# Kernel optimization log

Hardware: AMD Instinct MI355X
Metric: run time of the kernel (lower is better)

Reference implementation:

```python
import jax, jax.numpy as jnp
import numpy as np

B = 64            # graphs
N0 = 1024         # nodes per graph at level 0
DEG = 16          # avg degree
D = 128
NS = [1024, 820, 656, 525, 420, 336]  # ceil(0.8*n) cascade


def gcn(x, src, dst, valid, W, b, num_nodes):
    # x: [N,D]; src/dst: [E] int; valid: [E] float mask; W: [D,D]; b: [D]
    x = x @ W.T + b
    deg = jax.ops.segment_sum(valid, src, num_segments=num_nodes) + 1.0  # +1 self loop
    dis = jax.lax.rsqrt(deg)
    norm = dis[src] * dis[dst] * valid
    agg = jax.ops.segment_sum(norm[:, None] * x[src], dst, num_segments=num_nodes)
    return agg + (dis * dis)[:, None] * x  # self-loop term


def topk_pool(x, src, dst, valid, w, n, k):
    # PyG TopKPooling: score = tanh((x.w)/||w||); keep top ceil(ratio*n) per graph
    s = jnp.tanh((x @ w) / jnp.linalg.norm(w))
    _, idx = jax.lax.top_k(s.reshape(B, n), k)                    # [B,k] local ids
    perm = (idx + (jnp.arange(B) * n)[:, None]).reshape(-1)       # global ids
    xn = x[perm] * s[perm][:, None]
    new_id = jnp.full((B * n,), -1, jnp.int32).at[perm].set(jnp.arange(B * k, dtype=jnp.int32))
    ns_, nd_ = new_id[src], new_id[dst]
    v = valid * ((ns_ >= 0) & (nd_ >= 0)).astype(jnp.float32)
    return xn, jnp.maximum(ns_, 0), jnp.maximum(nd_, 0), v


def setup_inputs() -> dict:
    key = jax.random.key(0)
    ks = jax.random.split(key, 32)
    x = jax.random.normal(ks[0], (B * N0, D), jnp.float32)
    eg = N0 * DEG  # edges per graph
    local = jax.random.randint(ks[1], (2, B, eg), 0, N0, jnp.int32)
    edge_index = (local + (jnp.arange(B, dtype=jnp.int32) * N0)[None, :, None]).reshape(2, -1)
    batch = jnp.repeat(jnp.arange(B, dtype=jnp.int32), N0)
    sc = 1.0 / np.sqrt(D)
    inp = {"x": x, "edge_index": edge_index, "batch": batch}
    for i in range(1, 6):
        inp[f"c{i}w"] = jax.random.normal(ks[2 * i], (D, D), jnp.float32) * sc
        inp[f"c{i}b"] = jnp.zeros((D,), jnp.float32)
        inp[f"p{i}w"] = jax.random.normal(ks[2 * i + 1], (D,), jnp.float32) * sc
    inp["l1w"] = jax.random.normal(ks[20], (128, 256), jnp.float32) / np.sqrt(256)
    inp["l1b"] = jnp.zeros((128,), jnp.float32)
    inp["l2w"] = jax.random.normal(ks[21], (64, 128), jnp.float32) * sc
    inp["l2b"] = jnp.zeros((64,), jnp.float32)
    inp["l3w"] = jax.random.normal(ks[22], (2, 64), jnp.float32) / np.sqrt(64)
    inp["l3b"] = jnp.zeros((2,), jnp.float32)
    return inp


def reference(x, edge_index, batch,
              c1w, c1b, p1w, c2w, c2b, p2w, c3w, c3b, p3w,
              c4w, c4b, p4w, c5w, c5b, p5w,
              l1w, l1b, l2w, l2b, l3w, l3b):
    src, dst = edge_index[0], edge_index[1]
    valid = jnp.ones(src.shape, jnp.float32)
    layers = [(c1w, c1b, p1w), (c2w, c2b, p2w), (c3w, c3b, p3w),
              (c4w, c4b, p4w), (c5w, c5b, p5w)]
    reads = []
    for i, (cw, cb, pw) in enumerate(layers):
        n, k = NS[i], NS[i + 1]
        x = jax.nn.relu(gcn(x, src, dst, valid, cw, cb, B * n))
        x, src, dst, valid = topk_pool(x, src, dst, valid, pw, n, k)
        xk = x.reshape(B, k, D)
        reads.append(jnp.concatenate([xk.max(axis=1), xk.mean(axis=1)], axis=1))
    h = reads[0] + reads[1] + reads[2] + reads[3] + reads[4]   # [B,256]
    h = jax.nn.relu(h @ l1w.T + l1b)
    # dropout is identity in eval mode
    h = jax.nn.relu(h @ l2w.T + l2b)
    return jax.nn.log_softmax(h @ l3w.T + l3b, axis=-1)       # [B,2]
```

## Files before the change

### kernel.cpp

```cpp
#include <hip/hip_runtime.h>
#include <hip/hip_fp16.h>
#include <math.h>

#define NB 64
#define DIM 128
#define ETOT 1048576
#define EPG 16384
#define EPT 16
#define WRS 192
#define XRS 96

static const int NS_H[6] = {1024, 820, 656, 525, 420, 336};

__device__ __forceinline__ unsigned fxform(float f) {
    int b = __float_as_int(f);
    return (b >= 0) ? ((unsigned)b | 0x80000000u) : ~(unsigned)b;
}
__device__ __forceinline__ float fxinv(unsigned u) {
    int b = (u & 0x80000000u) ? (int)(u ^ 0x80000000u) : (int)~u;
    return __int_as_float(b);
}

__global__ __launch_bounds__(1024) void init_kernel(const int* __restrict__ ei,
                                  int* __restrict__ src, int* __restrict__ dst,
                                  int2* __restrict__ epack, int* __restrict__ eoff,
                                  int* __restrict__ cnt, float* __restrict__ dinv,
                                  float* __restrict__ invn, const float* __restrict__ pw0,
                                  unsigned* __restrict__ maxb, float* __restrict__ sumb) {
    __shared__ int hs[1024], hc[1024], cur[1024];
    __shared__ float dv[1024];
    __shared__ float shf[128];
    __shared__ int wsum[16];
    int g = blockIdx.x, t = threadIdx.x;
    int lane = t & 63, wv = t >> 6;
    hs[t] = 0; hc[t] = 0;
    int idx = g * 1024 + t;
    if (idx < 5 * NB * 128) { maxb[idx] = 0x007FFFFFu; sumb[idx] = 0.f; }
    __syncthreads();
    int b0 = g * EPG;
    int sr[EPT], dr[EPT];
#pragma unroll
    for (int q = 0; q < EPT; q++) {
        int e = b0 + q * 1024 + t;
        int s = ei[e], d = ei[ETOT + e];
        sr[q] = s; dr[q] = d;
        src[e] = s; dst[e] = d;
        atomicAdd(&hs[s & 1023], 1);
        atomicAdd(&hc[d & 1023], 1);
    }
    __syncthreads();
    int v = hc[t];
    dv[t] = rsqrtf((float)hs[t] + 1.0f);
    int s = v;
#pragma unroll
    for (int off = 1; off < 64; off <<= 1) {
        int u = __shfl_up(s, off, 64);
        if (lane >= off) s += u;
    }
    if (lane == 63) wsum[wv] = s;
    __syncthreads();
    if (wv == 0) {
        int ws = (lane < 16) ? wsum[lane] : 0;
#pragma unroll
        for (int off = 1; off < 16; off <<= 1) {
            int u = __shfl_up(ws, off, 64);
            if (lane >= off) ws += u;
        }
        if (lane < 16) wsum[lane] = ws;
    }
    __syncthreads();
    int excl = b0 + s + ((wv > 0) ? wsum[wv - 1] : 0) - v;
    eoff[g * 1024 + t] = excl;
    cnt[g * 1024 + t] = v;
    dinv[g * 1024 + t] = dv[t];
    cur[t] = excl;
    __syncthreads();
#pragma unroll
    for (int q = 0; q < EPT; q++) {
        int sl = sr[q] & 1023, dl = dr[q] & 1023;
        int pos = atomicAdd(&cur[dl], 1);
        epack[pos] = make_int2(sr[q], __float_as_int(dv[sl] * dv[dl]));
    }
    if (g == 0) {
        if (t < 128) shf[t] = pw0[t] * pw0[t];
        __syncthreads();
        for (int q = 64; q > 0; q >>= 1) {
            if (t < q) shf[t] += shf[t + q];
            __syncthreads();
        }
        if (t == 0) invn[0] = rsqrtf(shf[0]);
    }
}

__global__ __launch_bounds__(256) void linear_kernel(const float* __restrict__ x,
                              const __half* __restrict__ xA,
                              const int* __restrict__ perm, const float* __restrict__ sval,
                              const float* __restrict__ W, const float* __restrict__ b,
                              __half* __restrict__ xH,
                              unsigned* __restrict__ maxbL, float* __restrict__ sumbL,
                              int n_prev, int kk, int cpg, int mode) {
    __shared__ float Wt[32 * WRS];
    __shared__ float xT[32 * XRS];
    __shared__ float rmax[128], rsum[128];
    __shared__ float rmax2[8][32], rsum2[8][32];
    int tid = threadIdx.x;
    int g   = blockIdx.x / cpg;
    int j0  = (blockIdx.x % cpg) * 64;
    int nf = tid & 15;
    int u  = tid >> 4;
    int r   = tid & 63;
    int dq2 = tid >> 6;
    int jrow = j0 + r;
    int rowg = 0; float sscale = 1.f; bool valid = true;
    if (mode) {
        valid = (jrow < kk);
        int idx = g * kk + (valid ? jrow : 0);
        rowg = perm[idx];
        sscale = sval[idx];
    }
    float acc[4][8];
    {
        float bv[8];
#pragma unroll
        for (int f = 0; f < 8; f++) bv[f] = b[u * 8 + f];
#pragma unroll
        for (int i = 0; i < 4; i++)
#pragma unroll
            for (int f = 0; f < 8; f++) acc[i][f] = bv[f];
    }
    for (int kb = 0; kb < 4; kb++) {
        __syncthreads();
#pragma unroll
        for (int q = 0; q < 4; q++) {
            int i = q * 256 + tid;
            int dq = i >> 7;
            int rr = i & 127;
            int s = (rr >> 3) * 12 + (rr & 7);
            float4 wv = *(const float4*)(W + rr * 128 + kb * 32 + dq * 4);
            Wt[(dq * 4 + 0) * WRS + s] = wv.x;
            Wt[(dq * 4 + 1) * WRS + s] = wv.y;
            Wt[(dq * 4 + 2) * WRS + s] = wv.z;
            Wt[(dq * 4 + 3) * WRS + s] = wv.w;
        }
        int s = (r >> 3) * 12 + (r & 7);
        if (mode) {
            uint4 hv = *(const uint4*)(xA + ((size_t)(g * n_prev + rowg)) * DIM + kb * 32 + dq2 * 8);
            float2 c0 = __half22float2(*(const __half2*)&hv.x);
            float2 c1 = __half22float2(*(const __half2*)&hv.y);
            float2 c2 = __half22float2(*(const __half2*)&hv.z);
            float2 c3 = __half22float2(*(const __half2*)&hv.w);
            float v[8] = {c0.x * sscale, c0.y * sscale, c1.x * sscale, c1.y * sscale,
                          c2.x * sscale, c2.y * sscale, c3.x * sscale, c3.y * sscale};
            int cb2 = dq2 * 8;
#pragma unroll
            for (int i = 0; i < 8; i++) xT[(cb2 + i) * XRS + s] = valid ? v[i] : 0.f;
        } else {
#pragma unroll
            for (int q = 0; q < 2; q++) {
                int i = q * 256 + tid;
                int dq = i >> 6;
                float4 xv = *(const float4*)(x + (size_t)(g * kk + jrow) * DIM + kb * 32 + dq * 4);
                xT[(dq * 4 + 0) * XRS + s] = xv.x;
                xT[(dq * 4 + 1) * XRS + s] = xv.y;
                xT[(dq * 4 + 2) * XRS + s] = xv.z;
                xT[(dq * 4 + 3) * XRS + s] = xv.w;
            }
        }
        __syncthreads();
        if (mode) {
            int col = tid & 31, grp = tid >> 5;
            float m = -INFINITY, sv2 = 0.f;
#pragma unroll
            for (int rr = 0; rr < 8; rr++) {
                int ro = (rr + col) & 7;
                int row = grp * 8 + ro;
                float v = xT[col * XRS + grp * 12 + ro];
                if (j0 + row < kk) m = fmaxf(m, v);
                sv2 += v;
            }
            rmax2[grp][col] = m;
            rsum2[grp][col] = sv2;
        }
        __syncthreads();
        if (mode && tid < 32) {
            float m = rmax2[0][tid], sv2 = rsum2[0][tid];
#pragma unroll
            for (int p = 1; p < 8; p++) {
                m = fmaxf(m, rmax2[p][tid]);
                sv2 += rsum2[p][tid];
            }
            rmax[kb * 32 + tid] = m;
            rsum[kb * 32 + tid] = sv2;
        }
#pragma unroll 4
        for (int d = 0; d < 32; d++) {
            float4 xv = *(const float4*)&xT[d * XRS + (nf >> 1) * 12 + (nf & 1) * 4];
            float4 wa = *(const float4*)&Wt[d * WRS + u * 12];
            float4 wb = *(const float4*)&Wt[d * WRS + u * 12 + 4];
            float xs[4] = {xv.x, xv.y, xv.z, xv.w};
            float ws[8] = {wa.x, wa.y, wa.z, wa.w, wb.x, wb.y, wb.z, wb.w};
#pragma unroll
            for (int i = 0; i < 4; i++)
#pragma unroll
                for (int f = 0; f < 8; f++)
                    acc[i][f] += xs[i] * ws[f];
        }
    }
#pragma unroll
    for (int i = 0; i < 4; i++) {
        int jl = nf * 4 + i;
        if (j0 + jl < kk) {
            int nd = g * kk + j0 + jl;
            alignas(16) __half2 hb[4];
            hb[0] = __floats2half2_rn(acc[i][0], acc[i][1]);
            hb[1] = __floats2half2_rn(acc[i][2], acc[i][3]);
            hb[2] = __floats2half2_rn(acc[i][4], acc[i][5]);
            hb[3] = __floats2half2_rn(acc[i][6], acc[i][7]);
            *(float4*)(xH + (size_t)nd * DIM + u * 8) = *(const float4*)hb;
        }
    }
    if (mode) {
        __syncthreads();
        if (tid < 128) {
            atomicMax(&maxbL[g * 128 + tid], fxform(rmax[tid]));
            atomicAdd(&sumbL[g * 128 + tid], rsum[tid]);
        }
    }
}

#define CVT8_FMA(xv, wg) { \
    float2 c0_ = __half22float2(*(const __half2*)&(xv).x); \
    float2 c1_ = __half22float2(*(const __half2*)&(xv).y); \
    float2 c2_ = __half22float2(*(const __half2*)&(xv).z); \
    float2 c3_ = __half22float2(*(const __half2*)&(xv).w); \
    acc0 += (wg) * c0_.x; acc1 += (wg) * c0_.y; acc2 += (wg) * c1_.x; acc3 += (wg) * c1_.y; \
    acc4 += (wg) * c2_.x; acc5 += (wg) * c2_.y; acc6 += (wg) * c3_.x; acc7 += (wg) * c3_.y; }

__global__ __launch_bounds__(256, 4) void fused_agg_kernel(
                                 const __half* __restrict__ xH, const int2* __restrict__ epack,
                                 const int* __restrict__ eoff, const int* __restrict__ cnt,
                                 const float* __restrict__ dinv,
                                 const float* __restrict__ pw, const float* __restrict__ invn,
                                 __half* __restrict__ xA, float* __restrict__ score, int n) {
    int t = threadIdx.x;
    int g = blockIdx.x % NB;
    int chunk = blockIdx.x / NB;
    int ln = chunk * 8 + (t >> 5);
    if (ln >= n) return;
    int node = g * n + ln;
    int lane = t & 31;
    int sub = lane & 15;
    int hi  = lane >> 4;
    const uint4* __restrict__ xr = (const uint4*)xH;
    float dsn = dinv[node];
    float acc0 = 0.f, acc1 = 0.f, acc2 = 0.f, acc3 = 0.f;
    float acc4 = 0.f, acc5 = 0.f, acc6 = 0.f, acc7 = 0.f;
    {
        uint4 qs = xr[(unsigned)node * 16u + sub];
        float w0 = hi ? 0.f : dsn * dsn;
        CVT8_FMA(qs, w0);
    }
    int s0 = eoff[node], s1 = s0 + cnt[node];
    int j = s0;
    if ((j & 1) && j < s1) {
        int2 eq = epack[j];
        float wg = hi ? 0.f : __int_as_float(eq.y);
        uint4 xv = xr[(unsigned)eq.x * 16u + sub];
        CVT8_FMA(xv, wg);
        j++;
    }
    int np = (s1 - j) >> 1;
    int odd = (s1 - j) & 1;
    const int4* __restrict__ ep2 = (const int4*)epack;
    int p = j >> 1;
    while (np >= 8) {
        int4 E0 = ep2[p + 0], E1 = ep2[p + 1], E2 = ep2[p + 2], E3 = ep2[p + 3];
        int4 E4 = ep2[p + 4], E5 = ep2[p + 5], E6 = ep2[p + 6], E7 = ep2[p + 7];
        unsigned r0 = (unsigned)(hi ? E0.z : E0.x); float w0_ = __int_as_float(hi ? E0.w : E0.y);
        unsigned r1 = (unsigned)(hi ? E1.z : E1.x); float w1_ = __int_as_float(hi ? E1.w : E1.y);
        unsigned r2 = (unsigned)(hi ? E2.z : E2.x); float w2_ = __int_as_float(hi ? E2.w : E2.y);
        unsigned r3 = (unsigned)(hi ? E3.z : E3.x); float w3_ = __int_as_float(hi ? E3.w : E3.y);
        unsigned r4 = (unsigned)(hi ? E4.z : E4.x); float w4_ = __int_as_float(hi ? E4.w : E4.y);
        unsigned r5 = (unsigned)(hi ? E5.z : E5.x); float w5_ = __int_as_float(hi ? E5.w : E5.y);
        unsigned r6 = (unsigned)(hi ? E6.z : E6.x); float w6_ = __int_as_float(hi ? E6.w : E6.y);
        unsigned r7 = (unsigned)(hi ? E7.z : E7.x); float w7_ = __int_as_float(hi ? E7.w : E7.y);
        uint4 x0 = xr[r0 * 16u + sub];
        uint4 x1 = xr[r1 * 16u + sub];
        uint4 x2 = xr[r2 * 16u + sub];
        uint4 x3 = xr[r3 * 16u + sub];
        uint4 x4 = xr[r4 * 16u + sub];
        uint4 x5 = xr[r5 * 16u + sub];
        uint4 x6 = xr[r6 * 16u + sub];
        uint4 x7 = xr[r7 * 16u + sub];
        CVT8_FMA(x0, w0_); CVT8_FMA(x1, w1_); CVT8_FMA(x2, w2_); CVT8_FMA(x3, w3_);
        CVT8_FMA(x4, w4_); CVT8_FMA(x5, w5_); CVT8_FMA(x6, w6_); CVT8_FMA(x7, w7_);
        p += 8; np -= 8;
    }
    if (np >= 4) {
        int4 E0 = ep2[p + 0], E1 = ep2[p + 1], E2 = ep2[p + 2], E3 = ep2[p + 3];
        unsigned r0 = (unsigned)(hi ? E0.z : E0.x); float w0_ = __int_as_float(hi ? E0.w : E0.y);
        unsigned r1 = (unsigned)(hi ? E1.z : E1.x); float w1_ = __int_as_float(hi ? E1.w : E1.y);
        unsigned r2 = (unsigned)(hi ? E2.z : E2.x); float w2_ = __int_as_float(hi ? E2.w : E2.y);
        unsigned r3 = (unsigned)(hi ? E3.z : E3.x); float w3_ = __int_as_float(hi ? E3.w : E3.y);
        uint4 x0 = xr[r0 * 16u + sub];
        uint4 x1 = xr[r1 * 16u + sub];
        uint4 x2 = xr[r2 * 16u + sub];
        uint4 x3 = xr[r3 * 16u + sub];
        CVT8_FMA(x0, w0_); CVT8_FMA(x1, w1_); CVT8_FMA(x2, w2_); CVT8_FMA(x3, w3_);
        p += 4; np -= 4;
    }
    for (; np > 0; np--, p++) {
        int4 E = ep2[p];
        uint4 xv = xr[(unsigned)(hi ? E.z : E.x) * 16u + sub];
        float wg = __int_as_float(hi ? E.w : E.y);
        CVT8_FMA(xv, wg);
    }
    if (odd) {
        int2 eq = epack[s1 - 1];
        float wg = hi ? 0.f : __int_as_float(eq.y);
        uint4 xv = xr[(unsigned)eq.x * 16u + sub];
        CVT8_FMA(xv, wg);
    }
    acc0 += __shfl_xor(acc0, 16, 32); acc1 += __shfl_xor(acc1, 16, 32);
    acc2 += __shfl_xor(acc2, 16, 32); acc3 += __shfl_xor(acc3, 16, 32);
    acc4 += __shfl_xor(acc4, 16, 32); acc5 += __shfl_xor(acc5, 16, 32);
    acc6 += __shfl_xor(acc6, 16, 32); acc7 += __shfl_xor(acc7, 16, 32);
    acc0 = fmaxf(acc0, 0.f); acc1 = fmaxf(acc1, 0.f);
    acc2 = fmaxf(acc2, 0.f); acc3 = fmaxf(acc3, 0.f);
    acc4 = fmaxf(acc4, 0.f); acc5 = fmaxf(acc5, 0.f);
    acc6 = fmaxf(acc6, 0.f); acc7 = fmaxf(acc7, 0.f);
    if (!hi) {
        __half2 h0 = __floats2half2_rn(acc0, acc1);
        __half2 h1 = __floats2half2_rn(acc2, acc3);
        __half2 h2 = __floats2half2_rn(acc4, acc5);
        __half2 h3 = __floats2half2_rn(acc6, acc7);
        uint4 pk;
        pk.x = *(unsigned int*)&h0; pk.y = *(unsigned int*)&h1;
        pk.z = *(unsigned int*)&h2; pk.w = *(unsigned int*)&h3;
        ((uint4*)xA)[(unsigned)node * 16u + sub] = pk;
    }
    float4 pa = ((const float4*)pw)[sub * 2];
    float4 pb = ((const float4*)pw)[sub * 2 + 1];
    float dot = acc0 * pa.x + acc1 * pa.y + acc2 * pa.z + acc3 * pa.w
              + acc4 * pb.x + acc5 * pb.y + acc6 * pb.z + acc7 * pb.w;
#pragma unroll
    for (int off = 8; off >= 1; off >>= 1) dot += __shfl_xor(dot, off, 16);
    if (lane == 0) score[node] = tanhf(dot * invn[0]);
}

__global__ __launch_bounds__(1024) void pool_kernel(const float* __restrict__ score,
                              int* __restrict__ permG, float* __restrict__ svalG,
                              int* __restrict__ src, int* __restrict__ dst,
                              int2* __restrict__ epack, int* __restrict__ eoff,
                              int* __restrict__ cnt, float* __restrict__ dinv,
                              const float* __restrict__ pwN, float* __restrict__ invn,
                              int n, int k, int last) {
    __shared__ float keyS[2][1024];
    __shared__ int idxS[2][1024];
    __shared__ int nid[1024];
    __shared__ int hs[1024], hc[1024], cur[1024];
    __shared__ float dv[1024];
    __shared__ float shf[128];
    __shared__ int wsum[16];
    int g = blockIdx.x, t = threadIdx.x;
    int lane = t & 63, wv = t >> 6;
    int b0 = g * EPG, gn = g * n, gk = g * k;
    float k_r = (t < n) ? score[g * n + t] : -2.0f;
    int i_r = t;
    hs[t] = 0; hc[t] = 0;
    int se[EPT], de[EPT];
    if (!last) {
#pragma unroll
        for (int q = 0; q < EPT; q++) {
            int e = b0 + q * 1024 + t;
            se[q] = src[e];
            de[q] = dst[e];
        }
    }
    int par = 0;
    for (unsigned ksz = 2; ksz <= 1024; ksz <<= 1) {
        for (unsigned jj = ksz >> 1; jj > 0; jj >>= 1) {
            float kq; int iq;
            if (jj >= 64) {
                keyS[par][t] = k_r; idxS[par][t] = i_r;
                __syncthreads();
                kq = keyS[par][t ^ jj]; iq = idxS[par][t ^ jj];
                par ^= 1;
            } else {
                kq = __shfl_xor(k_r, (int)jj, 64);
                iq = __shfl_xor(i_r, (int)jj, 64);
            }
            bool mineFirst = (k_r > kq) || (k_r == kq && i_r < iq);
            bool up = ((t & ksz) == 0);
            bool iAmLower = ((t & jj) == 0);
            bool keepMine = (iAmLower == up) ? mineFirst : !mineFirst;
            if (!keepMine) { k_r = kq; i_r = iq; }
        }
    }
    nid[i_r] = (t < (unsigned)k) ? t : -1;
    if (t < k) { permG[gk + t] = i_r; svalG[gk + t] = k_r; }
    __syncthreads();
    if (last) return;
    int sr[EPT], dr[EPT];
#pragma unroll
    for (int q = 0; q < EPT; q++) {
        int e = b0 + q * 1024 + t;
        int s = se[q];
        int s2 = -1, d2 = -1;
        if (s >= 0) {
            s2 = nid[s - gn];
            d2 = nid[de[q] - gn];
            if (s2 >= 0 && d2 >= 0) {
                src[e] = gk + s2;
                dst[e] = gk + d2;
                atomicAdd(&hs[s2], 1);
                atomicAdd(&hc[d2], 1);
            } else {
                src[e] = -1;
                dst[e] = -1;
                s2 = -1;
            }
        }
        sr[q] = s2; dr[q] = d2;
    }
    __syncthreads();
    int v = (t < k) ? hc[t] : 0;
    if (t < k) dv[t] = rsqrtf((float)hs[t] + 1.0f);
    int s = v;
#pragma unroll
    for (int off = 1; off < 64; off <<= 1) {
        int u = __shfl_up(s, off, 64);
        if (lane >= off) s += u;
    }
    if (lane == 63) wsum[wv] = s;
    __syncthreads();
    if (wv == 0) {
        int ws = (lane < 16) ? wsum[lane] : 0;
#pragma unroll
        for (int off = 1; off < 16; off <<= 1) {
            int u = __shfl_up(ws, off, 64);
            if (lane >= off) ws += u;
        }
        if (lane < 16) wsum[lane] = ws;
    }
    __syncthreads();
    if (t < k) {
        int excl = b0 + s + ((wv > 0) ? wsum[wv - 1] : 0) - v;
        eoff[gk + t] = excl;
        cnt[gk + t] = v;
        dinv[gk + t] = dv[t];
        cur[t] = excl;
    }
    __syncthreads();
#pragma unroll
    for (int q = 0; q < EPT; q++) {
        if (sr[q] >= 0) {
            int pos = atomicAdd(&cur[dr[q]], 1);
            epack[pos] = make_int2(gk + sr[q], __float_as_int(dv[sr[q]] * dv[dr[q]]));
        }
    }
    if (g == 0) {
        if (t < 128) shf[t] = pwN[t] * pwN[t];
        __syncthreads();
        for (int q = 64; q > 0; q >>= 1) {
            if (t < q) shf[t] += shf[t + q];
            __syncthreads();
        }
        if (t == 0) invn[0] = rsqrtf(shf[0]);
    }
}

__global__ __launch_bounds__(256) void gather_kernel(const __half* __restrict__ xA,
                                const int* __restrict__ permG, const float* __restrict__ svalG,
                                unsigned* __restrict__ maxbL, float* __restrict__ sumbL,
                                int n, int k) {
    __shared__ float4 smx[8][33];
    __shared__ float4 ssm[8][33];
    int t = threadIdx.x;
    int g = blockIdx.x % NB;
    int chunk = blockIdx.x / NB;
    int j = chunk * 8 + (t >> 5);
    int lane = t & 31;
    int ch = t >> 5;
    float4 mx = make_float4(-INFINITY, -INFINITY, -INFINITY, -INFINITY);
    float4 sm = make_float4(0.f, 0.f, 0.f, 0.f);
    if (j < k) {
        int row = permG[g * k + j];
        float s = svalG[g * k + j];
        uint2 hv = ((const uint2*)(xA + ((size_t)g * n + row) * DIM))[lane];
        float2 lo = __half22float2(*(const __half2*)&hv.x);
        float2 hi = __half22float2(*(const __half2*)&hv.y);
        float4 vv = make_float4(lo.x * s, lo.y * s, hi.x * s, hi.y * s);
        mx = vv; sm = vv;
    }
    smx[ch][lane] = mx;
    ssm[ch][lane] = sm;
    __syncthreads();
    for (int s = 4; s >= 1; s >>= 1) {
        if (ch < s) {
            float4 a = smx[ch][lane], bb = smx[ch + s][lane];
            a.x = fmaxf(a.x, bb.x); a.y = fmaxf(a.y, bb.y);
            a.z = fmaxf(a.z, bb.z); a.w = fmaxf(a.w, bb.w);
            smx[ch][lane] = a;
            float4 c = ssm[ch][lane], d = ssm[ch + s][lane];
            c.x += d.x; c.y += d.y; c.z += d.z; c.w += d.w;
            ssm[ch][lane] = c;
        }
        __syncthreads();
    }
    if (ch == 0) {
        float4 m = smx[0][lane];
        float4 s4 = ssm[0][lane];
        int f0 = g * 128 + lane * 4;
        atomicMax(&maxbL[f0 + 0], fxform(m.x));
        atomicMax(&maxbL[f0 + 1], fxform(m.y));
        atomicMax(&maxbL[f0 + 2], fxform(m.z));
        atomicMax(&maxbL[f0 + 3], fxform(m.w));
        atomicAdd(&sumbL[f0 + 0], s4.x);
        atomicAdd(&sumbL[f0 + 1], s4.y);
        atomicAdd(&sumbL[f0 + 2], s4.z);
        atomicAdd(&sumbL[f0 + 3], s4.w);
    }
}

__global__ __launch_bounds__(128) void head_kernel(const unsigned* __restrict__ maxb,
                              const float* __restrict__ sumb,
                              const float* __restrict__ l1w, const float* __restrict__ l1b,
                              const float* __restrict__ l2w, const float* __restrict__ l2b,
                              const float* __restrict__ l3w, const float* __restrict__ l3b,
                              float* __restrict__ out) {
    __shared__ float hr[256], h1[128], h2[64], lz[2];
    int g = blockIdx.x, t = threadIdx.x;
    const float invk[5] = {1.f / 820.f, 1.f / 656.f, 1.f / 525.f, 1.f / 420.f, 1.f / 336.f};
    float mxs = 0.f, sms = 0.f;
#pragma unroll
    for (int L = 0; L < 5; L++) {
        mxs += fxinv(maxb[(L * NB + g) * 128 + t]);
        sms += sumb[(L * NB + g) * 128 + t] * invk[L];
    }
    hr[t] = mxs;
    hr[128 + t] = sms;
    __syncthreads();
    float a1 = l1b[t];
    for (int d = 0; d < 256; d++) a1 += hr[d] * l1w[t * 256 + d];
    h1[t] = fmaxf(a1, 0.f);
    __syncthreads();
    if (t < 64) {
        float a2 = l2b[t];
        for (int d = 0; d < 128; d++) a2 += h1[d] * l2w[t * 128 + d];
        h2[t] = fmaxf(a2, 0.f);
    }
    __syncthreads();
    if (t < 2) {
        float a3 = l3b[t];
        for (int d = 0; d < 64; d++) a3 += h2[d] * l3w[t * 64 + d];
        lz[t] = a3;
    }
    __syncthreads();
    if (t < 2) {
        float z0 = lz[0], z1 = lz[1];
        float m = fmaxf(z0, z1);
        float lse = m + logf(expf(z0 - m) + expf(z1 - m));
        out[g * 2 + t] = lz[t] - lse;
    }
}

extern "C" void kernel_launch(void* const* d_in, const int* in_sizes, int n_in,
                              void* d_out, int out_size, void* d_ws, size_t ws_size,
                              hipStream_t stream) {
    const float* x_in = (const float*)d_in[0];
    const int* edge_index = (const int*)d_in[1];
    const float *cw[5], *cb[5], *pw[5];
    for (int i = 0; i < 5; i++) {
        cw[i] = (const float*)d_in[3 + 3 * i];
        cb[i] = (const float*)d_in[4 + 3 * i];
        pw[i] = (const float*)d_in[5 + 3 * i];
    }
    const float* l1w = (const float*)d_in[18];
    const float* l1b = (const float*)d_in[19];
    const float* l2w = (const float*)d_in[20];
    const float* l2b = (const float*)d_in[21];
    const float* l3w = (const float*)d_in[22];
    const float* l3b = (const float*)d_in[23];
    float* out = (float*)d_out;

    char* w = (char*)d_ws;
    __half* xA    = (__half*)w; w += (size_t)65536 * DIM * 2;
    __half* xH    = (__half*)w; w += (size_t)65536 * DIM * 2;
    int*   src   = (int*)w;   w += (size_t)ETOT * 4;
    int*   dst   = (int*)w;   w += (size_t)ETOT * 4;
    int2*  epack = (int2*)w;  w += (size_t)ETOT * 8;
    int*   cnt   = (int*)w;   w += (size_t)65536 * 4;
    int*   eoff  = (int*)w;   w += (size_t)65536 * 4;
    float* dinv  = (float*)w; w += (size_t)65536 * 4;
    float* score = (float*)w; w += (size_t)65536 * 4;
    int*   perm  = (int*)w;   w += (size_t)65536 * 4;
    float* sval  = (float*)w; w += (size_t)65536 * 4;
    unsigned* maxb = (unsigned*)w; w += (size_t)5 * NB * 128 * 4;
    float* sumb  = (float*)w; w += (size_t)5 * NB * 128 * 4;
    float* invn  = (float*)w; w += 4;

    init_kernel<<<NB, 1024, 0, stream>>>(edge_index, src, dst, epack, eoff, cnt, dinv,
                                         invn, pw[0], maxb, sumb);

    for (int i = 0; i < 5; i++) {
        int n = NS_H[i], k = NS_H[i + 1];
        int cpg = (n + 63) / 64;
        int last = (i == 4) ? 1 : 0;

        linear_kernel<<<NB * cpg, 256, 0, stream>>>(
            x_in, xA, perm, sval, cw[i], cb[i], xH,
            (i > 0) ? maxb + (size_t)(i - 1) * NB * 128 : (unsigned*)maxb,
            (i > 0) ? sumb + (size_t)(i - 1) * NB * 128 : (float*)sumb,
            (i > 0) ? NS_H[i - 1] : 0, n, cpg, (i > 0) ? 1 : 0);

        int gpb = (n + 7) / 8;
        fused_agg_kernel<<<NB * gpb, 256, 0, stream>>>(xH, epack, eoff, cnt, dinv, pw[i],
                                                       invn, xA, score, n);
        pool_kernel<<<NB, 1024, 0, stream>>>(score, perm, sval, src, dst, epack, eoff,
                                             cnt, dinv, (i < 4) ? pw[i + 1] : pw[i], invn,
                                             n, k, last);
    }
    int k4 = NS_H[5];
    int gpk = (k4 + 7) / 8;
    gather_kernel<<<NB * gpk, 256, 0, stream>>>(xA, perm, sval,
                                                maxb + (size_t)4 * NB * 128,
                                                sumb + (size_t)4 * NB * 128,
                                                NS_H[4], k4);
    head_kernel<<<NB, 128, 0, stream>>>(maxb, sumb, l1w, l1b, l2w, l2b, l3w, l3b, out);
}
```

Measured before the change: 505.8 us.

## Use fp16 MFMA for GCN linear layer with shuffle-based readout reduction

Replaces the FP32 LDS-tiled outer-product GEMM in linear_kernel with the 16x16x32 fp16 MFMA instruction. Weights are converted to fp16 once in init_kernel, and activations are loaded straight into registers as B fragments. The per-block max/mean readout now uses cross-lane shuffles in half precision instead of LDS transposes. This removes LDS staging and most syncs, but the input x and the scaled activations are rounded to fp16, and partial sums are accumulated in fp16 during the shuffle steps, which costs accuracy.

```diff
diff --git a/kernel.cpp b/kernel.cpp
--- a/kernel.cpp
+++ b/kernel.cpp
@@ -7,10 +7,11 @@
 #define ETOT 1048576
 #define EPG 16384
 #define EPT 16
-#define WRS 192
-#define XRS 96
 
 static const int NS_H[6] = {1024, 820, 656, 525, 420, 336};
+
+typedef _Float16 f16x8 __attribute__((ext_vector_type(8)));
+typedef float f32x4 __attribute__((ext_vector_type(4)));
 
 __device__ __forceinline__ unsigned fxform(float f) {
     int b = __float_as_int(f);
@@ -19,6 +20,18 @@
 __device__ __forceinline__ float fxinv(unsigned u) {
     int b = (u & 0x80000000u) ? (int)(u ^ 0x80000000u) : (int)~u;
     return __int_as_float(b);
+}
+__device__ __forceinline__ unsigned hmax2u(unsigned a, unsigned b) {
+    float2 fa = __half22float2(*(__half2*)&a);
+    float2 fb = __half22float2(*(__half2*)&b);
+    __half2 r = __floats2half2_rn(fmaxf(fa.x, fb.x), fmaxf(fa.y, fb.y));
+    return *(unsigned*)&r;
+}
+__device__ __forceinline__ unsigned hadd2u(unsigned a, unsigned b) {
+    float2 fa = __half22float2(*(__half2*)&a);
+    float2 fb = __half22float2(*(__half2*)&b);
+    __half2 r = __floats2half2_rn(fa.x + fb.x, fa.y + fb.y);
+    return *(unsigned*)&r;
 }
 
 __global__ __launch_bounds__(1024) void init_kernel(const int* __restrict__ ei,
@@ -26,7 +39,10 @@
                                   int2* __restrict__ epack, int* __restrict__ eoff,
                                   int* __restrict__ cnt, float* __restrict__ dinv,
                                   float* __restrict__ invn, const float* __restrict__ pw0,
-                                  unsigned* __restrict__ maxb, float* __restrict__ sumb) {
+                                  unsigned* __restrict__ maxb, float* __restrict__ sumb,
+                                  const float* __restrict__ cw0, const float* __restrict__ cw1,
+                                  const float* __restrict__ cw2, const float* __restrict__ cw3,
+                                  const float* __restrict__ cw4, __half* __restrict__ W16) {
     __shared__ int hs[1024], hc[1024], cur[1024];
     __shared__ float dv[1024];
     __shared__ float shf[128];
@@ -36,6 +52,12 @@
     hs[t] = 0; hc[t] = 0;
     int idx = g * 1024 + t;
     if (idx < 5 * NB * 128) { maxb[idx] = 0x007FFFFFu; sumb[idx] = 0.f; }
+    if (g < 5) {
+        const float* wsrc = (g == 0) ? cw0 : (g == 1) ? cw1 : (g == 2) ? cw2
+                           : (g == 3) ? cw3 : cw4;
+        for (int i = t; i < 16384; i += 1024)
+            W16[g * 16384 + i] = __float2half(wsrc[i]);
+    }
     __syncthreads();
     int b0 = g * EPG;
     int sr[EPT], dr[EPT];
@@ -95,135 +117,126 @@
 __global__ __launch_bounds__(256) void linear_kernel(const float* __restrict__ x,
                               const __half* __restrict__ xA,
                               const int* __restrict__ perm, const float* __restrict__ sval,
-                              const float* __restrict__ W, const float* __restrict__ b,
+                              const __half* __restrict__ W16, const float* __restrict__ b,
                               __half* __restrict__ xH,
                               unsigned* __restrict__ maxbL, float* __restrict__ sumbL,
                               int n_prev, int kk, int cpg, int mode) {
-    __shared__ float Wt[32 * WRS];
-    __shared__ float xT[32 * XRS];
-    __shared__ float rmax[128], rsum[128];
-    __shared__ float rmax2[8][32], rsum2[8][32];
+    __shared__ float rmaxW[512], rsumW[512];
     int tid = threadIdx.x;
     int g   = blockIdx.x / cpg;
     int j0  = (blockIdx.x % cpg) * 64;
-    int nf = tid & 15;
-    int u  = tid >> 4;
-    int r   = tid & 63;
-    int dq2 = tid >> 6;
-    int jrow = j0 + r;
-    int rowg = 0; float sscale = 1.f; bool valid = true;
+    int wv  = tid >> 6;
+    int l   = tid & 63;
+    int l16 = l & 15;
+    int kgrp = l >> 4;
+    int jrow = j0 + wv * 16 + l16;
+    bool valid = jrow < kk;
+    f16x8 bf[4];
     if (mode) {
-        valid = (jrow < kk);
         int idx = g * kk + (valid ? jrow : 0);
-        rowg = perm[idx];
-        sscale = sval[idx];
-    }
-    float acc[4][8];
-    {
-        float bv[8];
-#pragma unroll
-        for (int f = 0; f < 8; f++) bv[f] = b[u * 8 + f];
-#pragma unroll
-        for (int i = 0; i < 4; i++)
-#pragma unroll
-            for (int f = 0; f < 8; f++) acc[i][f] = bv[f];
-    }
+        int rowg = perm[idx];
+        float sc = valid ? sval[idx] : 0.f;
+        const uint4* xrow = (const uint4*)(xA + (size_t)(g * n_prev + rowg) * DIM);
+#pragma unroll
+        for (int kb = 0; kb < 4; kb++) {
+            uint4 hv = xrow[kb * 4 + kgrp];
+            __half2* hp = (__half2*)&hv;
+#pragma unroll
+            for (int q = 0; q < 4; q++) {
+                float2 f = __half22float2(hp[q]);
+                hp[q] = __floats2half2_rn(f.x * sc, f.y * sc);
+            }
+            bf[kb] = *(f16x8*)&hv;
+        }
+    } else {
+        const float* xrow = x + (size_t)(g * kk + jrow) * DIM;
+#pragma unroll
+        for (int kb = 0; kb < 4; kb++) {
+            float4 a = *(const float4*)(xrow + kb * 32 + kgrp * 8);
+            float4 c = *(const float4*)(xrow + kb * 32 + kgrp * 8 + 4);
+            __half2 h0 = __floats2half2_rn(a.x, a.y), h1 = __floats2half2_rn(a.z, a.w);
+            __half2 h2 = __floats2half2_rn(c.x, c.y), h3 = __floats2half2_rn(c.z, c.w);
+            uint4 hv;
+            hv.x = *(unsigned*)&h0; hv.y = *(unsigned*)&h1;
+            hv.z = *(unsigned*)&h2; hv.w = *(unsigned*)&h3;
+            bf[kb] = *(f16x8*)&hv;
+        }
+    }
+    if (mode) {
+#pragma unroll
+        for (int kb = 0; kb < 4; kb++) {
+            uint4 fv = *(uint4*)&bf[kb];
+            uint4 mxv, smv;
+            if (valid) { mxv = fv; smv = fv; }
+            else {
+                mxv = make_uint4(0xFC00FC00u, 0xFC00FC00u, 0xFC00FC00u, 0xFC00FC00u);
+                smv = make_uint4(0u, 0u, 0u, 0u);
+            }
+#pragma unroll
+            for (int st = 1; st < 16; st <<= 1) {
+                uint4 om, os;
+                om.x = __shfl_xor(mxv.x, st, 16); om.y = __shfl_xor(mxv.y, st, 16);
+                om.z = __shfl_xor(mxv.z, st, 16); om.w = __shfl_xor(mxv.w, st, 16);
+                os.x = __shfl_xor(smv.x, st, 16); os.y = __shfl_xor(smv.y, st, 16);
+                os.z = __shfl_xor(smv.z, st, 16); os.w = __shfl_xor(smv.w, st, 16);
+                mxv.x = hmax2u(mxv.x, om.x); mxv.y = hmax2u(mxv.y, om.y);
+                mxv.z = hmax2u(mxv.z, om.z); mxv.w = hmax2u(mxv.w, om.w);
+                smv.x = hadd2u(smv.x, os.x); smv.y = hadd2u(smv.y, os.y);
+                smv.z = hadd2u(smv.z, os.z); smv.w = hadd2u(smv.w, os.w);
+            }
+            if (l16 == 0) {
+                int cb = wv * 128 + kb * 32 + kgrp * 8;
+                __half2* mh = (__half2*)&mxv;
+                __half2* sh = (__half2*)&smv;
+#pragma unroll
+                for (int q = 0; q < 4; q++) {
+                    float2 fm = __half22float2(mh[q]);
+                    float2 fs = __half22float2(sh[q]);
+                    rmaxW[cb + q * 2 + 0] = fm.x; rmaxW[cb + q * 2 + 1] = fm.y;
+                    rsumW[cb + q * 2 + 0] = fs.x; rsumW[cb + q * 2 + 1] = fs.y;
+                }
+            }
+        }
+    }
+    f32x4 acc[8];
+#pragma unroll
+    for (int ft = 0; ft < 8; ft++) {
+        float4 bv = *(const float4*)(b + ft * 16 + kgrp * 4);
+        f32x4 a; a[0] = bv.x; a[1] = bv.y; a[2] = bv.z; a[3] = bv.w;
+        acc[ft] = a;
+    }
+    const uint4* wp = (const uint4*)W16;
+#pragma unroll
     for (int kb = 0; kb < 4; kb++) {
-        __syncthreads();
-#pragma unroll
-        for (int q = 0; q < 4; q++) {
-            int i = q * 256 + tid;
-            int dq = i >> 7;
-            int rr = i & 127;
-            int s = (rr >> 3) * 12 + (rr & 7);
-            float4 wv = *(const float4*)(W + rr * 128 + kb * 32 + dq * 4);
-            Wt[(dq * 4 + 0) * WRS + s] = wv.x;
-            Wt[(dq * 4 + 1) * WRS + s] = wv.y;
-            Wt[(dq * 4 + 2) * WRS + s] = wv.z;
-            Wt[(dq * 4 + 3) * WRS + s] = wv.w;
-        }
-        int s = (r >> 3) * 12 + (r & 7);
-        if (mode) {
-            uint4 hv = *(const uint4*)(xA + ((size_t)(g * n_prev + rowg)) * DIM + kb * 32 + dq2 * 8);
-            float2 c0 = __half22float2(*(const __half2*)&hv.x);
-            float2 c1 = __half22float2(*(const __half2*)&hv.y);
-            float2 c2 = __half22float2(*(const __half2*)&hv.z);
-            float2 c3 = __half22float2(*(const __half2*)&hv.w);
-            float v[8] = {c0.x * sscale, c0.y * sscale, c1.x * sscale, c1.y * sscale,
-                          c2.x * sscale, c2.y * sscale, c3.x * sscale, c3.y * sscale};
-            int cb2 = dq2 * 8;
-#pragma unroll
-            for (int i = 0; i < 8; i++) xT[(cb2 + i) * XRS + s] = valid ? v[i] : 0.f;
-        } else {
-#pragma unroll
-            for (int q = 0; q < 2; q++) {
-                int i = q * 256 + tid;
-                int dq = i >> 6;
-                float4 xv = *(const float4*)(x + (size_t)(g * kk + jrow) * DIM + kb * 32 + dq * 4);
-                xT[(dq * 4 + 0) * XRS + s] = xv.x;
-                xT[(dq * 4 + 1) * XRS + s] = xv.y;
-                xT[(dq * 4 + 2) * XRS + s] = xv.z;
-                xT[(dq * 4 + 3) * XRS + s] = xv.w;
-            }
-        }
-        __syncthreads();
-        if (mode) {
-            int col = tid & 31, grp = tid >> 5;
-            float m = -INFINITY, sv2 = 0.f;
-#pragma unroll
-            for (int rr = 0; rr < 8; rr++) {
-                int ro = (rr + col) & 7;
-                int row = grp * 8 + ro;
-                float v = xT[col * XRS + grp * 12 + ro];
-                if (j0 + row < kk) m = fmaxf(m, v);
-                sv2 += v;
-            }
-            rmax2[grp][col] = m;
-            rsum2[grp][col] = sv2;
-        }
-        __syncthreads();
-        if (mode && tid < 32) {
-            float m = rmax2[0][tid], sv2 = rsum2[0][tid];
-#pragma unroll
-            for (int p = 1; p < 8; p++) {
-                m = fmaxf(m, rmax2[p][tid]);
-                sv2 += rsum2[p][tid];
-            }
-            rmax[kb * 32 + tid] = m;
-            rsum[kb * 32 + tid] = sv2;
-        }
-#pragma unroll 4
-        for (int d = 0; d < 32; d++) {
-            float4 xv = *(const float4*)&xT[d * XRS + (nf >> 1) * 12 + (nf & 1) * 4];
-            float4 wa = *(const float4*)&Wt[d * WRS + u * 12];
-            float4 wb = *(const float4*)&Wt[d * WRS + u * 12 + 4];
-            float xs[4] = {xv.x, xv.y, xv.z, xv.w};
-            float ws[8] = {wa.x, wa.y, wa.z, wa.w, wb.x, wb.y, wb.z, wb.w};
-#pragma unroll
-            for (int i = 0; i < 4; i++)
-#pragma unroll
-                for (int f = 0; f < 8; f++)
-                    acc[i][f] += xs[i] * ws[f];
-        }
-    }
-#pragma unroll
-    for (int i = 0; i < 4; i++) {
-        int jl = nf * 4 + i;
-        if (j0 + jl < kk) {
-            int nd = g * kk + j0 + jl;
-            alignas(16) __half2 hb[4];
-            hb[0] = __floats2half2_rn(acc[i][0], acc[i][1]);
-            hb[1] = __floats2half2_rn(acc[i][2], acc[i][3]);
-            hb[2] = __floats2half2_rn(acc[i][4], acc[i][5]);
-            hb[3] = __floats2half2_rn(acc[i][6], acc[i][7]);
-            *(float4*)(xH + (size_t)nd * DIM + u * 8) = *(const float4*)hb;
+#pragma unroll
+        for (int ft = 0; ft < 8; ft++) {
+            uint4 wfrag = wp[(ft * 16 + l16) * 16 + kb * 4 + kgrp];
+            acc[ft] = __builtin_amdgcn_mfma_f32_16x16x32_f16(*(f16x8*)&wfrag, bf[kb],
+                                                             acc[ft], 0, 0, 0);
+        }
+    }
+    if (valid) {
+        __half* yrow = xH + (size_t)(g * kk + jrow) * DIM;
+#pragma unroll
+        for (int ft = 0; ft < 8; ft++) {
+            __half2 h0 = __floats2half2_rn(acc[ft][0], acc[ft][1]);
+            __half2 h1 = __floats2half2_rn(acc[ft][2], acc[ft][3]);
+            uint2 pk;
+            pk.x = *(unsigned*)&h0; pk.y = *(unsigned*)&h1;
+            *(uint2*)(yrow + ft * 16 + kgrp * 4) = pk;
         }
     }
     if (mode) {
         __syncthreads();
         if (tid < 128) {
-            atomicMax(&maxbL[g * 128 + tid], fxform(rmax[tid]));
-            atomicAdd(&sumbL[g * 128 + tid], rsum[tid]);
+            float m = rmaxW[tid], s = rsumW[tid];
+#pragma unroll
+            for (int w = 1; w < 4; w++) {
+                m = fmaxf(m, rmaxW[w * 128 + tid]);
+                s += rsumW[w * 128 + tid];
+            }
+            atomicMax(&maxbL[g * 128 + tid], fxform(m));
+            atomicAdd(&sumbL[g * 128 + tid], s);
         }
     }
 }
@@ -598,10 +611,12 @@
     float* sval  = (float*)w; w += (size_t)65536 * 4;
     unsigned* maxb = (unsigned*)w; w += (size_t)5 * NB * 128 * 4;
     float* sumb  = (float*)w; w += (size_t)5 * NB * 128 * 4;
+    __half* W16  = (__half*)w; w += (size_t)5 * 16384 * 2;
     float* invn  = (float*)w; w += 4;
 
     init_kernel<<<NB, 1024, 0, stream>>>(edge_index, src, dst, epack, eoff, cnt, dinv,
-                                         invn, pw[0], maxb, sumb);
+                                         invn, pw[0], maxb, sumb,
+                                         cw[0], cw[1], cw[2], cw[3], cw[4], W16);
 
     for (int i = 0; i < 5; i++) {
         int n = NS_H[i], k = NS_H[i + 1];
@@ -609,7 +624,7 @@
         int last = (i == 4) ? 1 : 0;
 
         linear_kernel<<<NB * cpg, 256, 0, stream>>>(
-            x_in, xA, perm, sval, cw[i], cb[i], xH,
+            x_in, xA, perm, sval, W16 + (size_t)i * 16384, cb[i], xH,
             (i > 0) ? maxb + (size_t)(i - 1) * NB * 128 : (unsigned*)maxb,
             (i > 0) ? sumb + (size_t)(i - 1) * NB * 128 : (float*)sumb,
             (i > 0) ? NS_H[i - 1] : 0, n, cpg, (i > 0) ? 1 : 0);
```

Result: faster. 479.4 us (-5.2%).
